# Optimization experiments

Hardware: AMD Instinct MI355X
Metric: run time of the kernel (lower is better)

Reference implementation:

```python
import jax, jax.numpy as jnp
import numpy as np
import math

B, N, H, D = 1, 512, 8, 32
IN_DIM, EDGE_DIM = 128, 64
INNER = H * D


def setup_inputs() -> dict:
    key = jax.random.key(0)
    ks = jax.random.split(key, 11)
    s = 0.02
    return {
        "nodes": jax.random.normal(ks[0], (B, N, IN_DIM), jnp.float32),
        "edges": jax.random.normal(ks[1], (B, N, N, EDGE_DIM), jnp.float32),
        "adjacency": jax.random.randint(ks[2], (B, N, N), 0, 2, jnp.int32),
        "Wq": jax.random.normal(ks[3], (IN_DIM, INNER), jnp.float32) * s,
        "bq": jax.random.normal(ks[4], (INNER,), jnp.float32) * s,
        "Wk": jax.random.normal(ks[5], (IN_DIM, INNER), jnp.float32) * s,
        "bk": jax.random.normal(ks[6], (INNER,), jnp.float32) * s,
        "Wv": jax.random.normal(ks[7], (IN_DIM, INNER), jnp.float32) * s,
        "bv": jax.random.normal(ks[8], (INNER,), jnp.float32) * s,
        "We": jax.random.normal(ks[9], (EDGE_DIM, INNER), jnp.float32) * s,
        "be": jax.random.normal(ks[10], (INNER,), jnp.float32) * s,
    }


def _adj_softmax(x, adjacency):
    # Faithful to source quirk: torch.mean(x, -1, keepdim=True)[0] indexes
    # batch-head 0, giving per-row means of the first batch-head, shape (N, 1),
    # which then broadcasts over all batch-heads.
    means = jnp.mean(x, axis=-1, keepdims=True)[0]          # (N, 1)
    x_exp = jnp.exp(x - means) * adjacency                  # (BH, N, N)
    x_sum = jnp.sum(x_exp, axis=-1, keepdims=True)
    x_sum = jnp.where(x_sum == 0, 1.0, x_sum)
    return x_exp / x_sum


def reference(nodes, edges, adjacency, Wq, bq, Wk, bk, Wv, bv, We, be):
    b, n = nodes.shape[0], nodes.shape[1]
    # Projections
    q = nodes @ Wq + bq                                     # (b, n, H*D)
    k = nodes @ Wk + bk
    v = nodes @ Wv + bv
    e = edges @ We + be                                     # (b, n, n, H*D)
    # Split heads -> (b*H, n, D) and (b*H, n, n, D)
    q = q.reshape(b, n, H, D).transpose(0, 2, 1, 3).reshape(b * H, n, D)
    k = k.reshape(b, n, H, D).transpose(0, 2, 1, 3).reshape(b * H, n, D)
    v = v.reshape(b, n, H, D).transpose(0, 2, 1, 3).reshape(b * H, n, D)
    e = e.reshape(b, n, n, H, D).transpose(0, 3, 1, 2, 4).reshape(b * H, n, n, D)
    k_e = k[:, None, :, :] + e                              # (b*H, n, n, D)
    v_e = v[:, None, :, :] + e
    sim = jnp.einsum('bid,bijd->bij', q, k_e) / math.sqrt(D)
    adj = jnp.repeat(adjacency.astype(sim.dtype), H, axis=0)  # (b*H, n, n)
    attn = _adj_softmax(sim, adj)
    out = jnp.einsum('bij,bijd->bid', attn, v_e)            # (b*H, n, D)
    out = out.reshape(b, H, n, D).transpose(0, 2, 1, 3).reshape(b, n, H * D)
    return out
```

## Files before the change

### kernel.cpp

```cpp
#include <hip/hip_runtime.h>

#define N_NODES 512
#define INNER   256
#define IN_DIM  128
#define EDGE_DIM 64
#define NH 8
#define HD 32
#define SCALE 0.17677669529663687f

__global__ __launch_bounds__(256) void proj_qkv(
    const float* __restrict__ nodes,
    const float* __restrict__ Wq, const float* __restrict__ bq,
    const float* __restrict__ Wk, const float* __restrict__ bk,
    const float* __restrict__ Wv, const float* __restrict__ bv,
    float* __restrict__ q, float* __restrict__ k, float* __restrict__ v) {
  const int m  = blockIdx.x >> 6;
  const int i0 = (blockIdx.x & 63) * 8;
  const int n  = threadIdx.x;
  const float* __restrict__ W = (m == 0) ? Wq : (m == 1) ? Wk : Wv;
  const float* __restrict__ b = (m == 0) ? bq : (m == 1) ? bk : bv;
  float*       __restrict__ o = (m == 0) ? q  : (m == 1) ? k  : v;

  __shared__ float s_n[8 * IN_DIM];
  *(float4*)&s_n[n * 4] = *(const float4*)&nodes[(size_t)i0 * IN_DIM + n * 4];
  __syncthreads();

  float acc[8] = {0.f, 0.f, 0.f, 0.f, 0.f, 0.f, 0.f, 0.f};
#pragma unroll 4
  for (int c = 0; c < IN_DIM; ++c) {
    const float w = W[(size_t)c * INNER + n];
#pragma unroll
    for (int r = 0; r < 8; ++r) acc[r] = fmaf(s_n[r * IN_DIM + c], w, acc[r]);
  }
  const float bn = b[n];
#pragma unroll
  for (int r = 0; r < 8; ++r) o[(size_t)(i0 + r) * INNER + n] = acc[r] + bn;
}

__global__ __launch_bounds__(512) void qe_qb(
    const float* __restrict__ q, const float* __restrict__ We,
    const float* __restrict__ be,
    float* __restrict__ qe, float* __restrict__ qb) {
  const int i0  = blockIdx.x * 8;
  const int tid = threadIdx.x;

  __shared__ float s_q[8 * INNER];
  *(float4*)&s_q[tid * 4] = *(const float4*)&q[(size_t)i0 * INNER + tid * 4];
  __syncthreads();

  const int h = tid >> 6, c = tid & 63;
  float4 w[8];
#pragma unroll
  for (int d4 = 0; d4 < 8; ++d4)
    w[d4] = *(const float4*)&We[(size_t)c * INNER + h * HD + d4 * 4];

#pragma unroll
  for (int il = 0; il < 8; ++il) {
    const float* qh = &s_q[il * INNER + h * HD];
    float acc = 0.f;
#pragma unroll
    for (int d4 = 0; d4 < 8; ++d4) {
      const float4 q4 = *(const float4*)&qh[d4 * 4];
      acc += q4.x * w[d4].x + q4.y * w[d4].y + q4.z * w[d4].z + q4.w * w[d4].w;
    }
    qe[(size_t)(i0 + il) * (NH * EDGE_DIM) + h * EDGE_DIM + c] = acc;
  }

  if (tid < 64) {
    const int il = tid >> 3, h2 = tid & 7;
    float acc = 0.f;
    for (int d = 0; d < HD; ++d)
      acc += s_q[il * INNER + h2 * HD + d] * be[h2 * HD + d];
    qb[(size_t)(i0 + il) * NH + h2] = acc;
  }
}

__global__ __launch_bounds__(256) void qk_gemm(
    const float* __restrict__ q, const float* __restrict__ k,
    float* __restrict__ qk) {
  const int it = blockIdx.x >> 5, jt = blockIdx.x & 31;
  const int i0 = it * 16, j0 = jt * 16;
  const int tid = threadIdx.x;

  __shared__ float sq[16 * 260];
  __shared__ float sk[16 * 260];
#pragma unroll
  for (int p = 0; p < 4; ++p) {
    const int s = tid + p * 256;
    const int row = s >> 6, c4 = s & 63;
    *(float4*)&sq[row * 260 + c4 * 4] =
        *(const float4*)&q[(size_t)(i0 + row) * INNER + c4 * 4];
    *(float4*)&sk[row * 260 + c4 * 4] =
        *(const float4*)&k[(size_t)(j0 + row) * INNER + c4 * 4];
  }
  __syncthreads();

  const int il = tid >> 4, jl = tid & 15;
  float acc[NH];
#pragma unroll
  for (int h = 0; h < NH; ++h) {
    float s = 0.f;
#pragma unroll
    for (int d4 = 0; d4 < 8; ++d4) {
      const float4 q4 = *(const float4*)&sq[il * 260 + h * HD + d4 * 4];
      const float4 k4 = *(const float4*)&sk[jl * 260 + h * HD + d4 * 4];
      s += q4.x * k4.x + q4.y * k4.y + q4.z * k4.z + q4.w * k4.w;
    }
    acc[h] = s;
  }
#pragma unroll
  for (int h = 0; h < NH; ++h)
    qk[(size_t)(i0 + il) * (NH * N_NODES) + h * N_NODES + j0 + jl] = acc[h];
}

__global__ __launch_bounds__(512, 4) void fused_attn(
    const float* __restrict__ edges, const int* __restrict__ adjacency,
    const float* __restrict__ v,
    const float* __restrict__ qe, const float* __restrict__ qb,
    const float* __restrict__ qkbuf,
    const float* __restrict__ We, const float* __restrict__ be,
    float* __restrict__ out) {
  const int i   = blockIdx.x;
  const int tid = threadIdx.x;

  __shared__ float s_qe[NH * EDGE_DIM];
  __shared__ float s_qb[NH];
  __shared__ float s_adj[N_NODES];
  __shared__ float e_tile[128 * 68];
  __shared__ float p_lds[NH * 128];
  __shared__ float s_hred[8][2];
  __shared__ float s_rd[NH];
  __shared__ float s_as[NH];
  __shared__ float s_avp[2][INNER];
  __shared__ float s_ae[NH * EDGE_DIM];

  s_qe[tid]  = qe[(size_t)i * (NH * EDGE_DIM) + tid];
  s_adj[tid] = (float)adjacency[(size_t)i * N_NODES + tid];
  if (tid < NH) s_qb[tid] = qb[(size_t)i * NH + tid];

  const int j_l = tid & 127, hg = tid >> 7, h0 = hg * 2;
  const int cB  = tid & 63,  hB = tid >> 6;
  const int nC  = tid & 255, p2 = tid >> 8, hv = nC >> 5;

  float hs0 = 0.f, hs1 = 0.f, accv = 0.f, accae = 0.f;

  for (int jc = 0; jc < 4; ++jc) {
    __syncthreads();
    const float* esrc = edges + (size_t)i * (N_NODES * EDGE_DIM) + jc * (128 * EDGE_DIM);
#pragma unroll
    for (int p = 0; p < 4; ++p) {
      const int s = tid + p * 512;
      const int r = s >> 4, c4 = s & 15;
      *(float4*)&e_tile[r * 68 + c4 * 4] = *(const float4*)&esrc[s * 4];
    }
    __syncthreads();

    {
      const float* er  = &e_tile[j_l * 68];
      const float* qe0 = &s_qe[h0 * EDGE_DIM];
      const float* qe1 = qe0 + EDGE_DIM;
      float s0 = 0.f, s1 = 0.f;
#pragma unroll 4
      for (int c4 = 0; c4 < 16; ++c4) {
        const float4 e4 = *(const float4*)&er[c4 * 4];
        const float4 a0 = *(const float4*)&qe0[c4 * 4];
        const float4 a1 = *(const float4*)&qe1[c4 * 4];
        s0 += e4.x * a0.x + e4.y * a0.y + e4.z * a0.z + e4.w * a0.w;
        s1 += e4.x * a1.x + e4.y * a1.y + e4.z * a1.z + e4.w * a1.w;
      }
      const int jg = jc * 128 + j_l;
      const float qk0 = qkbuf[(size_t)i * (NH * N_NODES) + h0 * N_NODES + jg];
      const float qk1 = qkbuf[(size_t)i * (NH * N_NODES) + (h0 + 1) * N_NODES + jg];
      const float aj = s_adj[jg];
      const float p0 = __expf((s0 + qk0 + s_qb[h0]) * SCALE) * aj;
      const float p1 = __expf((s1 + qk1 + s_qb[h0 + 1]) * SCALE) * aj;
      p_lds[h0 * 128 + j_l]       = p0;
      p_lds[(h0 + 1) * 128 + j_l] = p1;
      hs0 += p0; hs1 += p1;
    }
    __syncthreads();

    {
      const float* pb = &p_lds[hB * 128];
      const float* eb = &e_tile[cB];
#pragma unroll 8
      for (int j4 = 0; j4 < 32; ++j4) {
        const float4 p4 = *(const float4*)&pb[j4 * 4];
        accae = fmaf(p4.x, eb[(j4 * 4 + 0) * 68], accae);
        accae = fmaf(p4.y, eb[(j4 * 4 + 1) * 68], accae);
        accae = fmaf(p4.z, eb[(j4 * 4 + 2) * 68], accae);
        accae = fmaf(p4.w, eb[(j4 * 4 + 3) * 68], accae);
      }
    }
    {
      const float* vc = v + (size_t)(jc * 128 + p2 * 64) * INNER + nC;
      const float* pr = &p_lds[hv * 128 + p2 * 64];
#pragma unroll 4
      for (int jj4 = 0; jj4 < 16; ++jj4) {
        const float4 p4 = *(const float4*)&pr[jj4 * 4];
        accv = fmaf(p4.x, vc[(size_t)(jj4 * 4 + 0) * INNER], accv);
        accv = fmaf(p4.y, vc[(size_t)(jj4 * 4 + 1) * INNER], accv);
        accv = fmaf(p4.z, vc[(size_t)(jj4 * 4 + 2) * INNER], accv);
        accv = fmaf(p4.w, vc[(size_t)(jj4 * 4 + 3) * INNER], accv);
      }
    }
  }

  {
    float a = hs0, b = hs1;
#pragma unroll
    for (int off = 32; off > 0; off >>= 1) {
      a += __shfl_xor(a, off, 64);
      b += __shfl_xor(b, off, 64);
    }
    if ((tid & 63) == 0) { s_hred[tid >> 6][0] = a; s_hred[tid >> 6][1] = b; }
  }
  s_avp[p2][nC] = accv;
  __syncthreads();
  if (tid < NH) {
    const int g = tid >> 1, r = tid & 1;
    const float t = s_hred[g * 2][r] + s_hred[g * 2 + 1][r];
    s_rd[tid] = (t == 0.f) ? 1.f : (1.f / t);
    s_as[tid] = (t == 0.f) ? 0.f : 1.f;
  }
  __syncthreads();

  s_ae[tid] = accae * s_rd[hB];
  __syncthreads();

  if (tid < INNER) {
    const int n = tid, h = n >> 5;
    float o = (s_avp[0][n] + s_avp[1][n]) * s_rd[h] + s_as[h] * be[n];
    const float* aeh = &s_ae[h * EDGE_DIM];
#pragma unroll 8
    for (int cc = 0; cc < EDGE_DIM; ++cc)
      o = fmaf(aeh[cc], We[(size_t)cc * INNER + n], o);
    out[(size_t)i * INNER + n] = o;
  }
}

extern "C" void kernel_launch(void* const* d_in, const int* in_sizes, int n_in,
                              void* d_out, int out_size, void* d_ws, size_t ws_size,
                              hipStream_t stream) {
  const float* nodes     = (const float*)d_in[0];
  const float* edges     = (const float*)d_in[1];
  const int*   adjacency = (const int*)d_in[2];
  const float* Wq = (const float*)d_in[3];
  const float* bq = (const float*)d_in[4];
  const float* Wk = (const float*)d_in[5];
  const float* bk = (const float*)d_in[6];
  const float* Wv = (const float*)d_in[7];
  const float* bv = (const float*)d_in[8];
  const float* We = (const float*)d_in[9];
  const float* be = (const float*)d_in[10];

  float* q   = (float*)d_ws;
  float* k   = q   + (size_t)N_NODES * INNER;
  float* v   = k   + (size_t)N_NODES * INNER;
  float* qe  = v   + (size_t)N_NODES * INNER;
  float* qb  = qe  + (size_t)N_NODES * NH * EDGE_DIM;
  float* qkb = qb  + (size_t)N_NODES * NH;

  proj_qkv<<<dim3(3 * 64), dim3(256), 0, stream>>>(
      nodes, Wq, bq, Wk, bk, Wv, bv, q, k, v);
  qe_qb<<<dim3(64), dim3(512), 0, stream>>>(q, We, be, qe, qb);
  qk_gemm<<<dim3(1024), dim3(256), 0, stream>>>(q, k, qkb);
  fused_attn<<<dim3(N_NODES), dim3(512), 0, stream>>>(
      edges, adjacency, v, qe, qb, qkb, We, be, (float*)d_out);
}
```

Measured before the change: 159.0 us.

## Accumulate p·edge products in registers from loaded edge values instead of LDS

Each thread now keeps the four edge float4s it loads from global memory in registers. It accumulates the attention-weighted edge sums for all 8 heads directly from them into 32 register accumulators, replacing the strided LDS column reads of the edge tile. The partial sums are reduced across lanes with shuffles and across waves through the reused edge tile in shared memory. The global loads are also issued before the barrier to overlap with prior work. This removes the LDS-bound accumulation loop and the separate s_ae buffer, at the cost of higher register pressure under launch bounds of 512 threads with 4 blocks and an extra cross-wave reduction.

```diff
diff --git a/kernel.cpp b/kernel.cpp
--- a/kernel.cpp
+++ b/kernel.cpp
@@ -123,40 +123,47 @@
   const int i   = blockIdx.x;
   const int tid = threadIdx.x;
 
+  __shared__ float u_tile[128 * 68];
+  __shared__ float p_lds[NH * 128];
   __shared__ float s_qe[NH * EDGE_DIM];
   __shared__ float s_qb[NH];
   __shared__ float s_adj[N_NODES];
-  __shared__ float e_tile[128 * 68];
-  __shared__ float p_lds[NH * 128];
   __shared__ float s_hred[8][2];
   __shared__ float s_rd[NH];
   __shared__ float s_as[NH];
   __shared__ float s_avp[2][INNER];
-  __shared__ float s_ae[NH * EDGE_DIM];
 
   s_qe[tid]  = qe[(size_t)i * (NH * EDGE_DIM) + tid];
   s_adj[tid] = (float)adjacency[(size_t)i * N_NODES + tid];
   if (tid < NH) s_qb[tid] = qb[(size_t)i * NH + tid];
 
+  const int rS  = tid >> 4,  cgS = tid & 15;
   const int j_l = tid & 127, hg = tid >> 7, h0 = hg * 2;
-  const int cB  = tid & 63,  hB = tid >> 6;
   const int nC  = tid & 255, p2 = tid >> 8, hv = nC >> 5;
 
-  float hs0 = 0.f, hs1 = 0.f, accv = 0.f, accae = 0.f;
+  float hs0 = 0.f, hs1 = 0.f, accv = 0.f;
+  float4 acc4[NH];
+#pragma unroll
+  for (int h = 0; h < NH; ++h) acc4[h] = make_float4(0.f, 0.f, 0.f, 0.f);
+
+  const float* ebase = edges + (size_t)i * (N_NODES * EDGE_DIM);
 
   for (int jc = 0; jc < 4; ++jc) {
+    const float* esrc = ebase + (size_t)jc * (128 * EDGE_DIM);
+    const float4 e0 = *(const float4*)&esrc[(size_t)(tid +    0) * 4];
+    const float4 e1 = *(const float4*)&esrc[(size_t)(tid +  512) * 4];
+    const float4 e2 = *(const float4*)&esrc[(size_t)(tid + 1024) * 4];
+    const float4 e3 = *(const float4*)&esrc[(size_t)(tid + 1536) * 4];
+
     __syncthreads();
-    const float* esrc = edges + (size_t)i * (N_NODES * EDGE_DIM) + jc * (128 * EDGE_DIM);
-#pragma unroll
-    for (int p = 0; p < 4; ++p) {
-      const int s = tid + p * 512;
-      const int r = s >> 4, c4 = s & 15;
-      *(float4*)&e_tile[r * 68 + c4 * 4] = *(const float4*)&esrc[s * 4];
-    }
+    *(float4*)&u_tile[(rS +  0) * 68 + cgS * 4] = e0;
+    *(float4*)&u_tile[(rS + 32) * 68 + cgS * 4] = e1;
+    *(float4*)&u_tile[(rS + 64) * 68 + cgS * 4] = e2;
+    *(float4*)&u_tile[(rS + 96) * 68 + cgS * 4] = e3;
     __syncthreads();
 
     {
-      const float* er  = &e_tile[j_l * 68];
+      const float* er  = &u_tile[j_l * 68];
       const float* qe0 = &s_qe[h0 * EDGE_DIM];
       const float* qe1 = qe0 + EDGE_DIM;
       float s0 = 0.f, s1 = 0.f;
@@ -180,18 +187,28 @@
     }
     __syncthreads();
 
-    {
-      const float* pb = &p_lds[hB * 128];
-      const float* eb = &e_tile[cB];
-#pragma unroll 8
-      for (int j4 = 0; j4 < 32; ++j4) {
-        const float4 p4 = *(const float4*)&pb[j4 * 4];
-        accae = fmaf(p4.x, eb[(j4 * 4 + 0) * 68], accae);
-        accae = fmaf(p4.y, eb[(j4 * 4 + 1) * 68], accae);
-        accae = fmaf(p4.z, eb[(j4 * 4 + 2) * 68], accae);
-        accae = fmaf(p4.w, eb[(j4 * 4 + 3) * 68], accae);
-      }
-    }
+#pragma unroll
+    for (int h = 0; h < NH; ++h) {
+      const float* ph = &p_lds[h * 128 + rS];
+      const float pa = ph[0], pb = ph[32], pc = ph[64], pd = ph[96];
+      acc4[h].x = fmaf(pa, e0.x, acc4[h].x);
+      acc4[h].y = fmaf(pa, e0.y, acc4[h].y);
+      acc4[h].z = fmaf(pa, e0.z, acc4[h].z);
+      acc4[h].w = fmaf(pa, e0.w, acc4[h].w);
+      acc4[h].x = fmaf(pb, e1.x, acc4[h].x);
+      acc4[h].y = fmaf(pb, e1.y, acc4[h].y);
+      acc4[h].z = fmaf(pb, e1.z, acc4[h].z);
+      acc4[h].w = fmaf(pb, e1.w, acc4[h].w);
+      acc4[h].x = fmaf(pc, e2.x, acc4[h].x);
+      acc4[h].y = fmaf(pc, e2.y, acc4[h].y);
+      acc4[h].z = fmaf(pc, e2.z, acc4[h].z);
+      acc4[h].w = fmaf(pc, e2.w, acc4[h].w);
+      acc4[h].x = fmaf(pd, e3.x, acc4[h].x);
+      acc4[h].y = fmaf(pd, e3.y, acc4[h].y);
+      acc4[h].z = fmaf(pd, e3.z, acc4[h].z);
+      acc4[h].w = fmaf(pd, e3.w, acc4[h].w);
+    }
+
     {
       const float* vc = v + (size_t)(jc * 128 + p2 * 64) * INNER + nC;
       const float* pr = &p_lds[hv * 128 + p2 * 64];
@@ -206,6 +223,26 @@
     }
   }
 
+#pragma unroll
+  for (int h = 0; h < NH; ++h) {
+    acc4[h].x += __shfl_xor(acc4[h].x, 16, 64);
+    acc4[h].y += __shfl_xor(acc4[h].y, 16, 64);
+    acc4[h].z += __shfl_xor(acc4[h].z, 16, 64);
+    acc4[h].w += __shfl_xor(acc4[h].w, 16, 64);
+    acc4[h].x += __shfl_xor(acc4[h].x, 32, 64);
+    acc4[h].y += __shfl_xor(acc4[h].y, 32, 64);
+    acc4[h].z += __shfl_xor(acc4[h].z, 32, 64);
+    acc4[h].w += __shfl_xor(acc4[h].w, 32, 64);
+  }
+  {
+    const int wv = tid >> 6;
+    if ((tid & 63) < 16) {
+#pragma unroll
+      for (int h = 0; h < NH; ++h)
+        *(float4*)&u_tile[wv * 512 + h * EDGE_DIM + cgS * 4] = acc4[h];
+    }
+  }
+
   {
     float a = hs0, b = hs1;
 #pragma unroll
@@ -225,13 +262,18 @@
   }
   __syncthreads();
 
-  s_ae[tid] = accae * s_rd[hB];
+  {
+    float t = 0.f;
+#pragma unroll
+    for (int w = 0; w < 8; ++w) t += u_tile[w * 512 + tid];
+    u_tile[4096 + tid] = t * s_rd[tid >> 6];
+  }
   __syncthreads();
 
   if (tid < INNER) {
     const int n = tid, h = n >> 5;
     float o = (s_avp[0][n] + s_avp[1][n]) * s_rd[h] + s_as[h] * be[n];
-    const float* aeh = &s_ae[h * EDGE_DIM];
+    const float* aeh = &u_tile[4096 + h * EDGE_DIM];
 #pragma unroll 8
     for (int cc = 0; cc < EDGE_DIM; ++cc)
       o = fmaf(aeh[cc], We[(size_t)cc * INNER + n], o);
```

Result: slower. 209.5 us (+31.8%).
